# Performance work log

Hardware: AMD Instinct MI355X
Metric: run time of the kernel (lower is better)

Reference implementation:

```python
import jax, jax.numpy as jnp
import numpy as np

B, T, C = 16, 1024, 128  # batch, block_size (window length), n_hembd


def setup_inputs() -> dict:
    key = jax.random.key(0)
    k1, k2, k3 = jax.random.split(key, 3)
    Q = jax.random.normal(k1, (B, T, C), dtype=jnp.float32)
    K = jax.random.normal(k2, (B, 2 * T - 1, C), dtype=jnp.float32)
    # learned parameter keyWindowBias: (1, 1, n_hembd, block_size)
    bias = jax.random.normal(k3, (1, 1, C, T), dtype=jnp.float32)
    return {"Q": Q, "K": K, "bias": bias}


def reference(Q, K, bias):
    # Original: K_sw = K.unfold(1, T, 1) -> (B, T, C, T) with K_sw[b,w,c,t] = K[b,w+t,c]
    #           Z = einsum('bwc,bwct->bwt', Q, K_sw + bias)
    # Distribute the dot product over the bias add to avoid materializing (B,T,C,T):
    #   Z[b,w,t] = sum_c Q[b,w,c] * K[b,w+t,c]  +  sum_c Q[b,w,c] * bias[c,t]
    Bn, Tn, Cn = Q.shape
    # Dense scores against all 2T-1 key positions: (B, T, 2T-1)
    S = jnp.einsum('bwc,bkc->bwk', Q, K)
    # Gather sliding-window diagonals: idx[w, t] = w + t
    idx = jnp.arange(Tn)[:, None] + jnp.arange(Tn)[None, :]  # (T, T)
    Zk = jnp.take_along_axis(S, idx[None, :, :], axis=2)      # (B, T, T)
    # Bias contribution: Q @ bias, shared across windows
    Zb = jnp.einsum('bwc,ct->bwt', Q, bias[0, 0])             # (B, T, T)
    return Zk + Zb
```

## Files before the change

### kernel.cpp

```cpp
#include <hip/hip_runtime.h>
#include <hip/hip_bf16.h>


#define B_    16
#define T_    1024
#define C_    128
#define KT_   2047

#define BW    32
#define BT    64
#define SS_LD 98

typedef unsigned short ushort_t;
typedef short bf16x8 __attribute__((ext_vector_type(8)));
typedef float f32x4  __attribute__((ext_vector_type(4)));
typedef float f32x16 __attribute__((ext_vector_type(16)));

__device__ __forceinline__ unsigned short f2bf(float f) {
  unsigned int u = __float_as_uint(f);
  u += 0x7FFFu + ((u >> 16) & 1u);
  return (unsigned short)(u >> 16);
}

typedef const __attribute__((address_space(1))) unsigned int* gas_ptr;
typedef __attribute__((address_space(3))) unsigned int* las_ptr;
__device__ __forceinline__ void async_copy16(const void* g, void* l) {
  __builtin_amdgcn_global_load_lds((gas_ptr)g, (las_ptr)l, 16, 0, 0);
}

__device__ __forceinline__ const bf16x8* frag(const ushort_t* t, int row, int kc) {
  return (const bf16x8*)(t + (((row << 4) + (kc ^ (row & 7))) << 3));
}

#define QN4 524288
#define KN4 1048064
#define BN4 32768

__global__ __launch_bounds__(256) void prepass(
    const float* __restrict__ Q, const float* __restrict__ K,
    const float* __restrict__ bias, ushort_t* __restrict__ Qb,
    ushort_t* __restrict__ Kb, ushort_t* __restrict__ bT) {
  int idx = blockIdx.x * 256 + threadIdx.x;
  if (idx < QN4) {
    float4 v = ((const float4*)Q)[idx];
    ((ushort4*)Qb)[idx] = make_ushort4(f2bf(v.x), f2bf(v.y), f2bf(v.z), f2bf(v.w));
  } else if (idx < QN4 + KN4) {
    int i = idx - QN4;
    float4 v = ((const float4*)K)[i];
    ((ushort4*)Kb)[i] = make_ushort4(f2bf(v.x), f2bf(v.y), f2bf(v.z), f2bf(v.w));
  } else if (idx < QN4 + KN4 + BN4) {
    int i = idx - (QN4 + KN4);
    int c = i >> 8;
    int g = i & 255;
    float4 v = ((const float4*)(bias + c * T_))[g];
    int t = g << 2;
    bT[(t + 0) * C_ + c] = f2bf(v.x);
    bT[(t + 1) * C_ + c] = f2bf(v.y);
    bT[(t + 2) * C_ + c] = f2bf(v.z);
    bT[(t + 3) * C_ + c] = f2bf(v.w);
  }
}

__global__ __launch_bounds__(320) void swmm_main(
    const ushort_t* __restrict__ Qb, const ushort_t* __restrict__ Kb,
    const ushort_t* __restrict__ bT, float* __restrict__ out) {
  __shared__ __align__(16) ushort_t tile[4096 * 8];
  __shared__ __align__(16) float Ss[BW * SS_LD];

  const int b     = blockIdx.z;
  const int wseg  = blockIdx.y;
  const int t0    = blockIdx.x * BT;
  const int wbase = wseg * 512;
  const int g0    = t0 + wbase;
  const int tid   = threadIdx.x;
  const int wv    = tid >> 6;
  const int lane  = tid & 63;
  const int lrow  = lane >> 4;
  const int p     = lane & 15;

  const ushort_t* Kbase = Kb + ((size_t)b * KT_) * C_;
  const ushort_t* Qbase = Qb + ((size_t)b * T_) * C_;

  for (int k = 0; k < 10; ++k) {
    int ch = k * 5 + wv;
    if (ch >= 48) break;
    if (ch < 24) {
      int r0 = ch * 4;
      int g  = g0 + r0 + lrow;
      int c  = p ^ (g & 7);
      int ga = g > KT_ - 1 ? KT_ - 1 : g;
      async_copy16(Kbase + (size_t)ga * C_ + (c << 3),
                   &tile[(size_t)(((g0 + r0) & 127) << 7)]);
    } else if (ch < 32) {
      int qr0 = (ch - 24) * 4;
      int qr  = qr0 + lrow;
      int c   = p ^ (qr & 7);
      async_copy16(Qbase + (size_t)(wbase + qr) * C_ + (c << 3),
                   &tile[(size_t)((128 + qr0) << 7)]);
    } else {
      int j0 = (ch - 32) * 4;
      int j  = j0 + lrow;
      int c  = p ^ (j & 7);
      async_copy16(bT + (size_t)(t0 + j) * C_ + (c << 3),
                   &tile[(size_t)((192 + j0) << 7)]);
    }
  }

  const int half = lane >> 5;
  const int l31  = lane & 31;

  for (int i = 0; i < 16; ++i) {
    const int w0 = wbase + (i << 5);
    const int gi = g0 + (i << 5);
    __syncthreads();

    if (i < 15) {
      for (int k = 0; k < 4; ++k) {
        int ch = k * 5 + wv;
        if (ch >= 16) break;
        if (ch < 8) {
          int qr0 = ch * 4;
          int qr  = qr0 + lrow;
          int c   = p ^ (qr & 7);
          async_copy16(Qbase + (size_t)(w0 + 32 + qr) * C_ + (c << 3),
                       &tile[(size_t)((128 + (((i + 1) & 1) << 5) + qr0) << 7)]);
        } else {
          int r0 = (ch - 8) * 4;
          int g  = gi + 96 + r0 + lrow;
          int c  = p ^ (g & 7);
          int ga = g > KT_ - 1 ? KT_ - 1 : g;
          async_copy16(Kbase + (size_t)ga * C_ + (c << 3),
                       &tile[(size_t)(((gi + 96 + r0) & 127) << 7)]);
        }
      }
    }

    const int Arow = 128 + ((i & 1) << 5) + l31;
    const int Brow = (wv < 3) ? ((gi + (wv << 5) + l31) & 127)
                              : (192 + ((wv - 3) << 5) + l31);
    f32x16 acc = {};
#pragma unroll
    for (int s = 0; s < 8; ++s) {
      int kc = 2 * s + half;
      bf16x8 a  = *frag(tile, Arow, kc);
      bf16x8 bb = *frag(tile, Brow, kc);
      acc = __builtin_amdgcn_mfma_f32_32x32x16_bf16(a, bb, acc, 0, 0, 0);
    }

    if (wv < 3) {
      int n0 = wv << 5;
#pragma unroll
      for (int r = 0; r < 16; ++r) {
        int row = (r & 3) + 8 * (r >> 2) + 4 * half;
        Ss[row * SS_LD + n0 + l31] = acc[r];
      }
    }
    __syncthreads();

    if (wv >= 3) {
      int j = ((wv - 3) << 5) + l31;
      float* orow = out + (size_t)(b * T_ + w0) * T_ + t0 + j;
#pragma unroll
      for (int r = 0; r < 16; ++r) {
        int irow = (r & 3) + 8 * (r >> 2) + 4 * half;
        orow[(size_t)irow * T_] = acc[r] + Ss[irow * SS_LD + irow + j];
      }
    }
  }
}

#define LDB 136
#define KROWS 96
__global__ __launch_bounds__(256) void swmm_fallback(
    const float* __restrict__ Q, const float* __restrict__ K,
    const float* __restrict__ bias, float* __restrict__ out) {
  __shared__ __align__(16) unsigned short Qs[BW * LDB];
  __shared__ __align__(16) unsigned short Ks[KROWS * LDB];
  __shared__ __align__(16) unsigned short Bs[BT * LDB];
  __shared__ __align__(16) float Ssf[BW * SS_LD];

  const int b   = blockIdx.z;
  const int w0  = blockIdx.y * BW;
  const int t0  = blockIdx.x * BT;
  const int kbase = w0 + t0;
  const int tid = threadIdx.x;

  {
    const float4* src = (const float4*)(Q + (size_t)(b * T_ + w0) * C_);
    for (int v = tid; v < BW * (C_ / 4); v += 256) {
      int r = v >> 5, cc = v & 31;
      float4 q = src[r * 32 + cc];
      unsigned short* d = &Qs[r * LDB + (cc << 2)];
      d[0] = f2bf(q.x); d[1] = f2bf(q.y); d[2] = f2bf(q.z); d[3] = f2bf(q.w);
    }
  }
  {
    for (int v = tid; v < KROWS * (C_ / 4); v += 256) {
      int r = v >> 5, cc = v & 31;
      int g = kbase + r;
      float4 kv = make_float4(0.f, 0.f, 0.f, 0.f);
      if (g < KT_) kv = ((const float4*)(K + ((size_t)b * KT_ + g) * C_))[cc];
      unsigned short* d = &Ks[r * LDB + (cc << 2)];
      d[0] = f2bf(kv.x); d[1] = f2bf(kv.y); d[2] = f2bf(kv.z); d[3] = f2bf(kv.w);
    }
  }
  {
    for (int v = tid; v < C_ * (BT / 4); v += 256) {
      int c = v >> 4, jj = v & 15;
      float4 bv = ((const float4*)(bias + (size_t)c * T_ + t0))[jj];
      int j4 = jj << 2;
      Bs[(j4 + 0) * LDB + c] = f2bf(bv.x);
      Bs[(j4 + 1) * LDB + c] = f2bf(bv.y);
      Bs[(j4 + 2) * LDB + c] = f2bf(bv.z);
      Bs[(j4 + 3) * LDB + c] = f2bf(bv.w);
    }
  }
  __syncthreads();

  const int wv    = tid >> 6;
  const int lane  = tid & 63;
  const int frow  = lane & 15;
  const int koff  = (lane >> 4) * 8;
  const int drow4 = (lane >> 4) * 4;
  const int NS = KROWS / 16;

  for (int s = wv; s < 2 * NS; s += 4) {
    int mb = s / NS, nn = s % NS;
    int m0 = mb * 16, nn0 = nn * 16;
    const unsigned short* arow = &Qs[(m0 + frow) * LDB + koff];
    const unsigned short* brow = &Ks[(nn0 + frow) * LDB + koff];
    f32x4 acc = {0.f, 0.f, 0.f, 0.f};
#pragma unroll
    for (int k0 = 0; k0 < C_; k0 += 32) {
      bf16x8 a  = *(const bf16x8*)(arow + k0);
      bf16x8 bb = *(const bf16x8*)(brow + k0);
      acc = __builtin_amdgcn_mfma_f32_16x16x32_bf16(a, bb, acc, 0, 0, 0);
    }
#pragma unroll
    for (int r = 0; r < 4; ++r)
      Ssf[(m0 + drow4 + r) * SS_LD + nn0 + frow] = acc[r];
  }

  f32x4 bacc[2];
#pragma unroll
  for (int q = 0; q < 2; ++q) {
    int idx = wv + q * 4;
    int m0 = (idx >> 2) * 16, j0 = (idx & 3) * 16;
    const unsigned short* arow = &Qs[(m0 + frow) * LDB + koff];
    const unsigned short* brow = &Bs[(j0 + frow) * LDB + koff];
    f32x4 acc = {0.f, 0.f, 0.f, 0.f};
#pragma unroll
    for (int k0 = 0; k0 < C_; k0 += 32) {
      bf16x8 a  = *(const bf16x8*)(arow + k0);
      bf16x8 bb = *(const bf16x8*)(brow + k0);
      acc = __builtin_amdgcn_mfma_f32_16x16x32_bf16(a, bb, acc, 0, 0, 0);
    }
    bacc[q] = acc;
  }
  __syncthreads();

#pragma unroll
  for (int q = 0; q < 2; ++q) {
    int idx = wv + q * 4;
    int m0 = (idx >> 2) * 16, j0 = (idx & 3) * 16;
#pragma unroll
    for (int r = 0; r < 4; ++r) {
      int i = m0 + drow4 + r;
      int j = j0 + frow;
      out[(size_t)(b * T_ + w0 + i) * T_ + t0 + j] = bacc[q][r] + Ssf[i * SS_LD + i + j];
    }
  }
}

extern "C" void kernel_launch(void* const* d_in, const int* in_sizes, int n_in,
                              void* d_out, int out_size, void* d_ws, size_t ws_size,
                              hipStream_t stream) {
  const float* Q    = (const float*)d_in[0];
  const float* K    = (const float*)d_in[1];
  const float* bias = (const float*)d_in[2];
  float* out = (float*)d_out;

  const size_t QB = (size_t)B_ * T_ * C_ * 2;
  const size_t KB = (size_t)B_ * KT_ * C_ * 2;
  const size_t TB = (size_t)T_ * C_ * 2;

  if (ws_size >= QB + KB + TB) {
    ushort_t* Qb = (ushort_t*)d_ws;
    ushort_t* Kb = (ushort_t*)((char*)d_ws + QB);
    ushort_t* bT = (ushort_t*)((char*)d_ws + QB + KB);
    prepass<<<(QN4 + KN4 + BN4) / 256, 256, 0, stream>>>(Q, K, bias, Qb, Kb, bT);
    swmm_main<<<dim3(T_ / BT, 2, B_), dim3(320), 0, stream>>>(Qb, Kb, bT, out);
  } else {
    swmm_fallback<<<dim3(T_ / BT, T_ / BW, B_), dim3(256), 0, stream>>>(Q, K, bias, out);
  }
}
```

Before: 134.7 us.

## Keep bias fragments in registers and software-pipeline the epilogue with one barrier

Bias-transposed fragments are loaded once into registers for the bias waves instead of being staged in shared memory, which shrinks the LDS tile. The S scratch buffer is double-buffered so each bias wave writes the output for the previous iteration while the K waves compute the current one, removing one __syncthreads per iteration. A final drain writes the last block. The aim is less barrier stall and better overlap of global stores with MFMA work, at the cost of more registers per bias wave (8 bf16x8 fragments plus a carried accumulator).

```diff
diff --git a/kernel.cpp b/kernel.cpp
--- a/kernel.cpp
+++ b/kernel.cpp
@@ -64,8 +64,8 @@
 __global__ __launch_bounds__(320) void swmm_main(
     const ushort_t* __restrict__ Qb, const ushort_t* __restrict__ Kb,
     const ushort_t* __restrict__ bT, float* __restrict__ out) {
-  __shared__ __align__(16) ushort_t tile[4096 * 8];
-  __shared__ __align__(16) float Ss[BW * SS_LD];
+  __shared__ __align__(16) ushort_t tile[192 * 128];
+  __shared__ __align__(16) float Ss[2][BW * SS_LD];
 
   const int b     = blockIdx.z;
   const int wseg  = blockIdx.y;
@@ -77,37 +77,40 @@
   const int lane  = tid & 63;
   const int lrow  = lane >> 4;
   const int p     = lane & 15;
-
-  const ushort_t* Kbase = Kb + ((size_t)b * KT_) * C_;
-  const ushort_t* Qbase = Qb + ((size_t)b * T_) * C_;
-
-  for (int k = 0; k < 10; ++k) {
+  const int half  = lane >> 5;
+  const int l31   = lane & 31;
+
+  const ushort_t* Kbase = Kb + (size_t)b * KT_ * C_;
+  const ushort_t* Qbase = Qb + (size_t)b * T_ * C_;
+
+  bf16x8 bfrag[8];
+  if (wv >= 3) {
+    const ushort_t* brow = bT + (size_t)(t0 + ((wv - 3) << 5) + l31) * C_;
+#pragma unroll
+    for (int s = 0; s < 8; ++s)
+      bfrag[s] = *(const bf16x8*)(brow + ((2 * s + half) << 3));
+  }
+
+  for (int k = 0; k < 7; ++k) {
     int ch = k * 5 + wv;
-    if (ch >= 48) break;
+    if (ch >= 32) break;
     if (ch < 24) {
       int r0 = ch * 4;
       int g  = g0 + r0 + lrow;
       int c  = p ^ (g & 7);
       int ga = g > KT_ - 1 ? KT_ - 1 : g;
       async_copy16(Kbase + (size_t)ga * C_ + (c << 3),
-                   &tile[(size_t)(((g0 + r0) & 127) << 7)]);
-    } else if (ch < 32) {
+                   &tile[(size_t)((g0 + r0) & 127) << 7]);
+    } else {
       int qr0 = (ch - 24) * 4;
       int qr  = qr0 + lrow;
       int c   = p ^ (qr & 7);
       async_copy16(Qbase + (size_t)(wbase + qr) * C_ + (c << 3),
-                   &tile[(size_t)((128 + qr0) << 7)]);
-    } else {
-      int j0 = (ch - 32) * 4;
-      int j  = j0 + lrow;
-      int c  = p ^ (j & 7);
-      async_copy16(bT + (size_t)(t0 + j) * C_ + (c << 3),
-                   &tile[(size_t)((192 + j0) << 7)]);
-    }
-  }
-
-  const int half = lane >> 5;
-  const int l31  = lane & 31;
+                   &tile[(size_t)(128 + qr0) << 7]);
+    }
+  }
+
+  f32x16 pacc = {};
 
   for (int i = 0; i < 16; ++i) {
     const int w0 = wbase + (i << 5);
@@ -123,48 +126,67 @@
           int qr  = qr0 + lrow;
           int c   = p ^ (qr & 7);
           async_copy16(Qbase + (size_t)(w0 + 32 + qr) * C_ + (c << 3),
-                       &tile[(size_t)((128 + (((i + 1) & 1) << 5) + qr0) << 7)]);
+                       &tile[(size_t)(128 + (((i + 1) & 1) << 5) + qr0) << 7]);
         } else {
           int r0 = (ch - 8) * 4;
           int g  = gi + 96 + r0 + lrow;
           int c  = p ^ (g & 7);
           int ga = g > KT_ - 1 ? KT_ - 1 : g;
           async_copy16(Kbase + (size_t)ga * C_ + (c << 3),
-                       &tile[(size_t)(((gi + 96 + r0) & 127) << 7)]);
+                       &tile[(size_t)((gi + 96 + r0) & 127) << 7]);
         }
       }
     }
 
     const int Arow = 128 + ((i & 1) << 5) + l31;
-    const int Brow = (wv < 3) ? ((gi + (wv << 5) + l31) & 127)
-                              : (192 + ((wv - 3) << 5) + l31);
-    f32x16 acc = {};
-#pragma unroll
-    for (int s = 0; s < 8; ++s) {
-      int kc = 2 * s + half;
-      bf16x8 a  = *frag(tile, Arow, kc);
-      bf16x8 bb = *frag(tile, Brow, kc);
-      acc = __builtin_amdgcn_mfma_f32_32x32x16_bf16(a, bb, acc, 0, 0, 0);
-    }
 
     if (wv < 3) {
-      int n0 = wv << 5;
+      const int Brow = (gi + (wv << 5) + l31) & 127;
+      f32x16 acc = {};
+#pragma unroll
+      for (int s = 0; s < 8; ++s) {
+        int kc = 2 * s + half;
+        acc = __builtin_amdgcn_mfma_f32_32x32x16_bf16(
+            *frag(tile, Arow, kc), *frag(tile, Brow, kc), acc, 0, 0, 0);
+      }
+      const int n0 = wv << 5;
+      float* Sd = Ss[i & 1];
 #pragma unroll
       for (int r = 0; r < 16; ++r) {
         int row = (r & 3) + 8 * (r >> 2) + 4 * half;
-        Ss[row * SS_LD + n0 + l31] = acc[r];
-      }
-    }
-    __syncthreads();
-
-    if (wv >= 3) {
-      int j = ((wv - 3) << 5) + l31;
-      float* orow = out + (size_t)(b * T_ + w0) * T_ + t0 + j;
-#pragma unroll
-      for (int r = 0; r < 16; ++r) {
-        int irow = (r & 3) + 8 * (r >> 2) + 4 * half;
-        orow[(size_t)irow * T_] = acc[r] + Ss[irow * SS_LD + irow + j];
-      }
+        Sd[row * SS_LD + n0 + l31] = acc[r];
+      }
+    } else {
+      if (i > 0) {
+        const float* Sp = Ss[(i - 1) & 1];
+        const int j = ((wv - 3) << 5) + l31;
+        float* orow = out + (size_t)(b * T_ + (w0 - 32)) * T_ + t0 + j;
+#pragma unroll
+        for (int r = 0; r < 16; ++r) {
+          int irow = (r & 3) + 8 * (r >> 2) + 4 * half;
+          orow[(size_t)irow * T_] = pacc[r] + Sp[irow * SS_LD + irow + j];
+        }
+      }
+      f32x16 acc = {};
+#pragma unroll
+      for (int s = 0; s < 8; ++s) {
+        int kc = 2 * s + half;
+        acc = __builtin_amdgcn_mfma_f32_32x32x16_bf16(
+            *frag(tile, Arow, kc), bfrag[s], acc, 0, 0, 0);
+      }
+      pacc = acc;
+    }
+  }
+
+  __syncthreads();
+  if (wv >= 3) {
+    const float* Sp = Ss[1];
+    const int j = ((wv - 3) << 5) + l31;
+    float* orow = out + (size_t)(b * T_ + wbase + 480) * T_ + t0 + j;
+#pragma unroll
+    for (int r = 0; r < 16; ++r) {
+      int irow = (r & 3) + 8 * (r >> 2) + 4 * half;
+      orow[(size_t)irow * T_] = pacc[r] + Sp[irow * SS_LD + irow + j];
     }
   }
 }
```

Result: faster. 127.4 us (-5.4%).
